# Performance work log

Measured on AMD Instinct MI355X. Metric: run time of the kernel, lower is better.

## Reference

```python
import jax, jax.numpy as jnp
import numpy as np


def _grid_sample_3d(vol, grid):
    """Trilinear 3D grid_sample, zero padding, align_corners=False (torch default).

    vol:  [B, C, D, H, W]
    grid: [B, P, 3] normalized coords in [-1, 1]; grid[...,0]->W axis,
          grid[...,1]->H axis, grid[...,2]->D axis (torch convention).
    returns [B, C, P]
    """
    B, C, D, H, W = vol.shape
    x = (grid[..., 0] + 1.0) * (W * 0.5) - 0.5
    y = (grid[..., 1] + 1.0) * (H * 0.5) - 0.5
    z = (grid[..., 2] + 1.0) * (D * 0.5) - 0.5
    x0, y0, z0 = jnp.floor(x), jnp.floor(y), jnp.floor(z)
    gather = jax.vmap(lambda v, zz, yy, xx: v[:, zz, yy, xx])  # per-batch gather -> [C, P]
    out = jnp.zeros((B, C, x.shape[1]), vol.dtype)
    for dz in (0.0, 1.0):
        for dy in (0.0, 1.0):
            for dx in (0.0, 1.0):
                xi, yi, zi = x0 + dx, y0 + dy, z0 + dz
                w = (1.0 - jnp.abs(x - xi)) * (1.0 - jnp.abs(y - yi)) * (1.0 - jnp.abs(z - zi))
                valid = (xi >= 0) & (xi < W) & (yi >= 0) & (yi < H) & (zi >= 0) & (zi < D)
                xc = jnp.clip(xi, 0, W - 1).astype(jnp.int32)
                yc = jnp.clip(yi, 0, H - 1).astype(jnp.int32)
                zc = jnp.clip(zi, 0, D - 1).astype(jnp.int32)
                vals = gather(vol, zc, yc, xc)  # [B, C, P]
                out = out + vals * jnp.where(valid, w, 0.0)[:, None, :]
    return out


def _offset_grid(xs, A, Wk):
    """xs: [N,3] sample points; A: [N,3,3]; Wk: [3,K] offset weights.
    Returns [N, K, 3] grid coords ordered (z_feat, y_feat, x_feat) as in the torch code."""
    off = jnp.einsum('nij,jk->nik', A, Wk)  # bmm with repeated weight -> [N,3,K]
    xf = xs[:, 2:3] + off[:, 0, :]
    yf = xs[:, 1:2] + off[:, 1, :]
    zf = xs[:, 0:1] + off[:, 2, :]
    return jnp.stack([zf, yf, xf], axis=-1)


def setup_inputs() -> dict:
    key = jax.random.key(0)
    k1, k2, k3, k4 = jax.random.split(key, 4)
    B, C, D, H, W = 2, 16, 96, 96, 96
    Feats, K = 512, 1024
    inp = jax.random.normal(k1, (B, C, D, H, W), jnp.float32)
    xyz_sample = jax.random.uniform(k2, (B, Feats, 3), jnp.float32, -1.0, 1.0)
    A = jax.random.normal(k3, (B * Feats, 3, 3), jnp.float32) * 0.1
    weight = jax.random.normal(k4, (6, K), jnp.float32) * 0.05  # xyz_off.weight
    return {"input": inp, "xyz_sample": xyz_sample, "A": A, "weight": weight}


def reference(input, xyz_sample, A, weight):
    B, Feats, _ = xyz_sample.shape
    C = input.shape[1]
    K = weight.shape[1]  # 1024
    xs = xyz_sample.reshape(B * Feats, 3)
    g1 = _offset_grid(xs, A, weight[:3]).reshape(B, Feats * K, 3)
    g2 = _offset_grid(xs, A, weight[3:]).reshape(B, Feats * K, 3)
    feats = _grid_sample_3d(input, g1) - _grid_sample_3d(input, g2)  # [B, C, Feats*K]
    return feats.reshape(B, C * Feats, K)
```

## Files before the change

### kernel.cpp

```cpp
#include <hip/hip_runtime.h>


#define NB 2
#define NC 16
#define NS 96
#define FEATS 512
#define NK 1024
#define KSPLIT 4
#define KSHIFT 2
#define KCHUNK (NK / KSPLIT)
#define DPASSES (KCHUNK / 128)

#define RVOX 8
#define VSTRIDE 48

#define TP 388

__device__ __forceinline__ unsigned int bfround(float f) {
  unsigned int u = __float_as_uint(f);
  return (u + 0x7fffu + ((u >> 16) & 1u)) >> 16;
}

__global__ __launch_bounds__(256) void transpose_bf16_kernel(
    const float* __restrict__ vol, unsigned short* __restrict__ volT) {
  int bid = blockIdx.x;
  int hq = bid % 24;
  int t = bid / 24;
  int d = t % NS;
  int b = t / NS;

  __shared__ float sm[NC * TP];
  int tid = threadIdx.x;

  const float4* v4 = (const float4*)vol;
#pragma unroll
  for (int j = 0; j < 6; j++) {
    int i = tid + 256 * j;
    int c = i / 96;
    int u = i - c * 96;
    size_t src = (size_t)((b * NC + c) * NS + d) * 2304 + hq * 96 + u;
    *(float4*)&sm[c * TP + u * 4] = v4[src];
  }
  __syncthreads();

  size_t dstb = ((size_t)(b * NS + d) * 9216 + (size_t)hq * 384) * NC;
#pragma unroll
  for (int j = 0; j < 3; j++) {
    int m = tid + 256 * j;
    int t16 = m >> 1;
    int ch = m & 1;
    unsigned int r[4];
#pragma unroll
    for (int q = 0; q < 4; q++) {
      float lo = sm[(ch * 8 + 2 * q) * TP + t16];
      float hi = sm[(ch * 8 + 2 * q + 1) * TP + t16];
      r[q] = bfround(lo) | (bfround(hi) << 16);
    }
    *(uint4*)(volT + dstb + (size_t)m * 8) = make_uint4(r[0], r[1], r[2], r[3]);
  }
}

#define BLO(v) __uint_as_float((v) << 16)
#define BHI(v) __uint_as_float((v) & 0xffff0000u)

__device__ __forceinline__ void tri_duo(
    const unsigned short* __restrict__ vg,
    size_t bbase,
    const unsigned char* __restrict__ sp,
    int ox0, int oy0, int oz0,
    float x, float y, float z, float sgn, float acc[8]) {
  float fx0 = floorf(x), fy0 = floorf(y), fz0 = floorf(z);
  int ix0 = (int)fx0, iy0 = (int)fy0, iz0 = (int)fz0;
  float tx = x - fx0, ty = y - fy0, tz = z - fz0;
  float wxa[2] = {1.0f - tx, tx};
  float wya[2] = {1.0f - ty, ty};
  float wza[2] = {1.0f - tz, tz};

  int lx0 = ix0 - ox0, ly0 = iy0 - oy0, lz0 = iz0 - oz0;
  bool fast = ((unsigned)lx0 < 7u) & ((unsigned)ly0 < 7u) & ((unsigned)lz0 < 7u);

  if (__builtin_expect(fast, 1)) {
#pragma unroll
    for (int dz = 0; dz < 2; dz++) {
      float wz = sgn * wza[dz];
#pragma unroll
      for (int dy = 0; dy < 2; dy++) {
        float wzy = wz * wya[dy];
        const unsigned char* rp =
            sp + (((lz0 + dz) * RVOX + (ly0 + dy)) * RVOX + lx0) * VSTRIDE;
#pragma unroll
        for (int dx = 0; dx < 2; dx++) {
          float w = wzy * wxa[dx];
          uint4 u = *(const uint4*)(rp + dx * VSTRIDE);
          acc[0] += w * BLO(u.x);
          acc[1] += w * BHI(u.x);
          acc[2] += w * BLO(u.y);
          acc[3] += w * BHI(u.y);
          acc[4] += w * BLO(u.z);
          acc[5] += w * BHI(u.z);
          acc[6] += w * BLO(u.w);
          acc[7] += w * BHI(u.w);
        }
      }
    }
  } else {
#pragma unroll
    for (int dz = 0; dz < 2; dz++) {
      int zc = iz0 + dz;
      if ((unsigned)zc >= (unsigned)NS) continue;
#pragma unroll
      for (int dy = 0; dy < 2; dy++) {
        int yc = iy0 + dy;
        if ((unsigned)yc >= (unsigned)NS) continue;
        size_t rowb = bbase + ((size_t)zc * NS + yc) * (NS * NC);
        float wzy = sgn * wza[dz] * wya[dy];
#pragma unroll
        for (int dx = 0; dx < 2; dx++) {
          int xc = ix0 + dx;
          if ((unsigned)xc >= (unsigned)NS) continue;
          float w = wzy * wxa[dx];
          uint4 u = *(const uint4*)(vg + rowb + (size_t)xc * NC);
          acc[0] += w * BLO(u.x);
          acc[1] += w * BHI(u.x);
          acc[2] += w * BLO(u.y);
          acc[3] += w * BHI(u.y);
          acc[4] += w * BLO(u.z);
          acc[5] += w * BHI(u.z);
          acc[6] += w * BLO(u.w);
          acc[7] += w * BHI(u.w);
        }
      }
    }
  }
}

__global__ __launch_bounds__(256) void sample_kernel_q(
    const unsigned short* __restrict__ volT,
    const float* __restrict__ xyz, const float* __restrict__ A,
    const float* __restrict__ weight, float* __restrict__ out) {
  __shared__ float wsm[6 * KCHUNK];
  __shared__ __align__(16) unsigned char stage[RVOX * RVOX * RVOX * VSTRIDE];

  int bid = blockIdx.x;
  int kseg = bid & (KSPLIT - 1);
  int n = bid >> KSHIFT;
  int b = n >> 9;
  int f = n & 511;
  int kbase = kseg * KCHUNK;

  for (int i = threadIdx.x; i < 6 * KCHUNK; i += 256)
    wsm[i] = weight[(i / KCHUNK) * NK + kbase + (i % KCHUNK)];

  const float* An = A + (size_t)n * 9;
  float a00 = An[0], a01 = An[1], a02 = An[2];
  float a10 = An[3], a11 = An[4], a12 = An[5];
  float a20 = An[6], a21 = An[7], a22 = An[8];
  const float* Xn = xyz + (size_t)n * 3;
  float bx = (Xn[0] + 1.0f) * 48.0f - 0.5f;
  float by = (Xn[1] + 1.0f) * 48.0f - 0.5f;
  float bz = (Xn[2] + 1.0f) * 48.0f - 0.5f;

  int ox0 = (int)floorf(bx) - 3;
  int oy0 = (int)floorf(by) - 3;
  int oz0 = (int)floorf(bz) - 3;

  size_t bbase = (size_t)b * (NS * NS * NS * NC);

  for (int v = threadIdx.x; v < RVOX * RVOX * RVOX; v += 256) {
    int dx = v & 7, dy = (v >> 3) & 7, dz = v >> 6;
    int xc = ox0 + dx, yc = oy0 + dy, zc = oz0 + dz;
    uint4 lo = make_uint4(0u, 0u, 0u, 0u);
    uint4 hi = make_uint4(0u, 0u, 0u, 0u);
    if (((unsigned)xc < (unsigned)NS) & ((unsigned)yc < (unsigned)NS) &
        ((unsigned)zc < (unsigned)NS)) {
      const uint4* g = (const uint4*)(volT + bbase +
                                      (((size_t)zc * NS + yc) * NS + xc) * NC);
      lo = g[0];
      hi = g[1];
    }
    unsigned char* p = stage + (size_t)v * VSTRIDE;
    *(uint4*)p = lo;
    *(uint4*)(p + 16) = hi;
  }
  __syncthreads();

  int duo = threadIdx.x & 1;
  int ksub = threadIdx.x >> 1;
  const unsigned short* vg = volT + duo * 8;
  const unsigned char* sp = stage + duo * 16;
  size_t obase = (size_t)b * (NC * FEATS * NK) +
                 (size_t)(duo * 8) * (FEATS * NK) + (size_t)f * NK + kbase;

  for (int pass = 0; pass < DPASSES; pass++) {
    int kl = pass * 128 + ksub;
    float w0 = wsm[kl];
    float w1 = wsm[KCHUNK + kl];
    float w2 = wsm[2 * KCHUNK + kl];
    float w3 = wsm[3 * KCHUNK + kl];
    float w4 = wsm[4 * KCHUNK + kl];
    float w5 = wsm[5 * KCHUNK + kl];

    float acc[8] = {0.0f, 0.0f, 0.0f, 0.0f, 0.0f, 0.0f, 0.0f, 0.0f};

    {
      float oz = a00 * w0 + a01 * w1 + a02 * w2;
      float oy = a10 * w0 + a11 * w1 + a12 * w2;
      float ox = a20 * w0 + a21 * w1 + a22 * w2;
      tri_duo(vg, bbase, sp, ox0, oy0, oz0, bx + ox * 48.0f, by + oy * 48.0f,
              bz + oz * 48.0f, 1.0f, acc);
    }
    {
      float oz = a00 * w3 + a01 * w4 + a02 * w5;
      float oy = a10 * w3 + a11 * w4 + a12 * w5;
      float ox = a20 * w3 + a21 * w4 + a22 * w5;
      tri_duo(vg, bbase, sp, ox0, oy0, oz0, bx + ox * 48.0f, by + oy * 48.0f,
              bz + oz * 48.0f, -1.0f, acc);
    }

    size_t o = obase + kl;
#pragma unroll
    for (int c = 0; c < 8; c++)
      out[o + (size_t)c * (FEATS * NK)] = acc[c];
  }
}

__global__ __launch_bounds__(256) void sample_kernel_fallback(
    const float* __restrict__ vol, const float* __restrict__ xyz,
    const float* __restrict__ A, const float* __restrict__ weight,
    float* __restrict__ out) {
  int n = blockIdx.x;
  int b = n >> 9;
  int f = n & 511;
  const float* An = A + (size_t)n * 9;
  float a00 = An[0], a01 = An[1], a02 = An[2];
  float a10 = An[3], a11 = An[4], a12 = An[5];
  float a20 = An[6], a21 = An[7], a22 = An[8];
  const float* Xn = xyz + (size_t)n * 3;
  float bx = (Xn[0] + 1.0f) * 48.0f - 0.5f;
  float by = (Xn[1] + 1.0f) * 48.0f - 0.5f;
  float bz = (Xn[2] + 1.0f) * 48.0f - 0.5f;
  size_t obase = (size_t)b * (NC * FEATS * NK) + (size_t)f * NK;

  for (int k = threadIdx.x; k < NK; k += 256) {
    float w0 = weight[k], w1 = weight[NK + k], w2 = weight[2 * NK + k];
    float w3 = weight[3 * NK + k], w4 = weight[4 * NK + k],
          w5 = weight[5 * NK + k];
    float acc[NC];
#pragma unroll
    for (int c = 0; c < NC; c++) acc[c] = 0.0f;
    for (int g = 0; g < 2; g++) {
      float u0 = g ? w3 : w0, u1 = g ? w4 : w1, u2 = g ? w5 : w2;
      float sgn = g ? -1.0f : 1.0f;
      float oz = a00 * u0 + a01 * u1 + a02 * u2;
      float oy = a10 * u0 + a11 * u1 + a12 * u2;
      float ox = a20 * u0 + a21 * u1 + a22 * u2;
      float x = bx + ox * 48.0f, y = by + oy * 48.0f, z = bz + oz * 48.0f;
      float fx0 = floorf(x), fy0 = floorf(y), fz0 = floorf(z);
      int ix0 = (int)fx0, iy0 = (int)fy0, iz0 = (int)fz0;
      float tx = x - fx0, ty = y - fy0, tz = z - fz0;
      float wxa[2] = {1.0f - tx, tx}, wya[2] = {1.0f - ty, ty},
            wza[2] = {1.0f - tz, tz};
      for (int dz = 0; dz < 2; dz++) {
        int zc = iz0 + dz;
        if ((unsigned)zc >= (unsigned)NS) continue;
        for (int dy = 0; dy < 2; dy++) {
          int yc = iy0 + dy;
          if ((unsigned)yc >= (unsigned)NS) continue;
          for (int dx = 0; dx < 2; dx++) {
            int xc = ix0 + dx;
            if ((unsigned)xc >= (unsigned)NS) continue;
            float w = sgn * wza[dz] * wya[dy] * wxa[dx];
            size_t base = (size_t)b * NC * NS * NS * NS +
                          (size_t)zc * NS * NS + (size_t)yc * NS + xc;
#pragma unroll
            for (int c = 0; c < NC; c++)
              acc[c] += w * vol[base + (size_t)c * (NS * NS * NS)];
          }
        }
      }
    }
#pragma unroll
    for (int c = 0; c < NC; c++)
      out[obase + (size_t)c * (FEATS * NK) + k] = acc[c];
  }
}

extern "C" void kernel_launch(void* const* d_in, const int* in_sizes, int n_in,
                              void* d_out, int out_size, void* d_ws,
                              size_t ws_size, hipStream_t stream) {
  const float* vol    = (const float*)d_in[0];
  const float* xyz    = (const float*)d_in[1];
  const float* A      = (const float*)d_in[2];
  const float* weight = (const float*)d_in[3];
  float* out = (float*)d_out;

  const size_t volT_bytes =
      (size_t)NB * NC * NS * NS * NS * sizeof(unsigned short);

  if (ws_size >= volT_bytes) {
    unsigned short* volT = (unsigned short*)d_ws;
    transpose_bf16_kernel<<<NB * NS * 24, 256, 0, stream>>>(vol, volT);
    sample_kernel_q<<<NB * FEATS * KSPLIT, 256, 0, stream>>>(volT, xyz, A,
                                                             weight, out);
  } else {
    sample_kernel_fallback<<<NB * FEATS, 256, 0, stream>>>(vol, xyz, A, weight,
                                                           out);
  }
}
```

Measured before the change: 223.9 us.

## Fuse volume transpose into sampler, staging bf16 neighborhood directly from fp32 input

Drops the separate full-volume transpose/bf16 conversion kernel. Each block now gathers its 8x8x8 voxel neighborhood straight from the channel-major fp32 volume, converts it to bf16 in shared memory, and falls back to fp32 global reads when a sample lands outside the stage. KSPLIT is halved to 2 so each block covers more K and amortizes staging, and the offset weights are loaded into registers instead of shared memory. The goal is to avoid the transpose's full-volume read and write; the cost is strided channel gathers (eight loads per voxel at stride NS^3) and fewer, longer blocks.

```diff
diff --git a/kernel.cpp b/kernel.cpp
--- a/kernel.cpp
+++ b/kernel.cpp
@@ -4,68 +4,26 @@
 #define NB 2
 #define NC 16
 #define NS 96
+#define NS3 (NS * NS * NS)
 #define FEATS 512
 #define NK 1024
-#define KSPLIT 4
-#define KSHIFT 2
+#define KSPLIT 2
 #define KCHUNK (NK / KSPLIT)
-#define DPASSES (KCHUNK / 128)
+#define PASSES 4
 
 #define RVOX 8
 #define VSTRIDE 48
-
-#define TP 388
 
 __device__ __forceinline__ unsigned int bfround(float f) {
   unsigned int u = __float_as_uint(f);
   return (u + 0x7fffu + ((u >> 16) & 1u)) >> 16;
 }
 
-__global__ __launch_bounds__(256) void transpose_bf16_kernel(
-    const float* __restrict__ vol, unsigned short* __restrict__ volT) {
-  int bid = blockIdx.x;
-  int hq = bid % 24;
-  int t = bid / 24;
-  int d = t % NS;
-  int b = t / NS;
-
-  __shared__ float sm[NC * TP];
-  int tid = threadIdx.x;
-
-  const float4* v4 = (const float4*)vol;
-#pragma unroll
-  for (int j = 0; j < 6; j++) {
-    int i = tid + 256 * j;
-    int c = i / 96;
-    int u = i - c * 96;
-    size_t src = (size_t)((b * NC + c) * NS + d) * 2304 + hq * 96 + u;
-    *(float4*)&sm[c * TP + u * 4] = v4[src];
-  }
-  __syncthreads();
-
-  size_t dstb = ((size_t)(b * NS + d) * 9216 + (size_t)hq * 384) * NC;
-#pragma unroll
-  for (int j = 0; j < 3; j++) {
-    int m = tid + 256 * j;
-    int t16 = m >> 1;
-    int ch = m & 1;
-    unsigned int r[4];
-#pragma unroll
-    for (int q = 0; q < 4; q++) {
-      float lo = sm[(ch * 8 + 2 * q) * TP + t16];
-      float hi = sm[(ch * 8 + 2 * q + 1) * TP + t16];
-      r[q] = bfround(lo) | (bfround(hi) << 16);
-    }
-    *(uint4*)(volT + dstb + (size_t)m * 8) = make_uint4(r[0], r[1], r[2], r[3]);
-  }
-}
-
 #define BLO(v) __uint_as_float((v) << 16)
 #define BHI(v) __uint_as_float((v) & 0xffff0000u)
 
 __device__ __forceinline__ void tri_duo(
-    const unsigned short* __restrict__ vg,
-    size_t bbase,
+    const float* __restrict__ vol, size_t cbase,
     const unsigned char* __restrict__ sp,
     int ox0, int oy0, int oz0,
     float x, float y, float z, float sgn, float acc[8]) {
@@ -112,93 +70,104 @@
       for (int dy = 0; dy < 2; dy++) {
         int yc = iy0 + dy;
         if ((unsigned)yc >= (unsigned)NS) continue;
-        size_t rowb = bbase + ((size_t)zc * NS + yc) * (NS * NC);
         float wzy = sgn * wza[dz] * wya[dy];
 #pragma unroll
         for (int dx = 0; dx < 2; dx++) {
           int xc = ix0 + dx;
           if ((unsigned)xc >= (unsigned)NS) continue;
           float w = wzy * wxa[dx];
-          uint4 u = *(const uint4*)(vg + rowb + (size_t)xc * NC);
-          acc[0] += w * BLO(u.x);
-          acc[1] += w * BHI(u.x);
-          acc[2] += w * BLO(u.y);
-          acc[3] += w * BHI(u.y);
-          acc[4] += w * BLO(u.z);
-          acc[5] += w * BHI(u.z);
-          acc[6] += w * BLO(u.w);
-          acc[7] += w * BHI(u.w);
+          const float* p = vol + cbase + (((size_t)zc * NS + yc) * NS + xc);
+#pragma unroll
+          for (int c = 0; c < 8; c++)
+            acc[c] += w * p[(size_t)c * NS3];
         }
       }
     }
   }
 }
 
-__global__ __launch_bounds__(256) void sample_kernel_q(
-    const unsigned short* __restrict__ volT,
-    const float* __restrict__ xyz, const float* __restrict__ A,
-    const float* __restrict__ weight, float* __restrict__ out) {
-  __shared__ float wsm[6 * KCHUNK];
+__global__ __launch_bounds__(256) void sample_fused(
+    const float* __restrict__ vol, const float* __restrict__ xyz,
+    const float* __restrict__ A, const float* __restrict__ weight,
+    float* __restrict__ out) {
   __shared__ __align__(16) unsigned char stage[RVOX * RVOX * RVOX * VSTRIDE];
 
   int bid = blockIdx.x;
   int kseg = bid & (KSPLIT - 1);
-  int n = bid >> KSHIFT;
+  int n = bid >> 1;
   int b = n >> 9;
   int f = n & 511;
   int kbase = kseg * KCHUNK;
-
-  for (int i = threadIdx.x; i < 6 * KCHUNK; i += 256)
-    wsm[i] = weight[(i / KCHUNK) * NK + kbase + (i % KCHUNK)];
+  int tid = threadIdx.x;
+
+  const float* Xn = xyz + (size_t)n * 3;
+  float bx = (Xn[0] + 1.0f) * 48.0f - 0.5f;
+  float by = (Xn[1] + 1.0f) * 48.0f - 0.5f;
+  float bz = (Xn[2] + 1.0f) * 48.0f - 0.5f;
+  int ox0 = (int)floorf(bx) - 3;
+  int oy0 = (int)floorf(by) - 3;
+  int oz0 = (int)floorf(bz) - 3;
+
+  int duo = tid & 1;
+  int ksub = tid >> 1;
+
+  float wreg[PASSES][6];
+#pragma unroll
+  for (int p = 0; p < PASSES; p++) {
+    int k = kbase + p * 128 + ksub;
+#pragma unroll
+    for (int q = 0; q < 6; q++) wreg[p][q] = weight[q * NK + k];
+  }
 
   const float* An = A + (size_t)n * 9;
   float a00 = An[0], a01 = An[1], a02 = An[2];
   float a10 = An[3], a11 = An[4], a12 = An[5];
   float a20 = An[6], a21 = An[7], a22 = An[8];
-  const float* Xn = xyz + (size_t)n * 3;
-  float bx = (Xn[0] + 1.0f) * 48.0f - 0.5f;
-  float by = (Xn[1] + 1.0f) * 48.0f - 0.5f;
-  float bz = (Xn[2] + 1.0f) * 48.0f - 0.5f;
-
-  int ox0 = (int)floorf(bx) - 3;
-  int oy0 = (int)floorf(by) - 3;
-  int oz0 = (int)floorf(bz) - 3;
-
-  size_t bbase = (size_t)b * (NS * NS * NS * NC);
-
-  for (int v = threadIdx.x; v < RVOX * RVOX * RVOX; v += 256) {
-    int dx = v & 7, dy = (v >> 3) & 7, dz = v >> 6;
-    int xc = ox0 + dx, yc = oy0 + dy, zc = oz0 + dz;
-    uint4 lo = make_uint4(0u, 0u, 0u, 0u);
-    uint4 hi = make_uint4(0u, 0u, 0u, 0u);
+
+  size_t vb = (size_t)b * NC * NS3;
+#pragma unroll
+  for (int j = 0; j < 4; j++) {
+    int w = tid + 256 * j;
+    int half = w & 1;
+    int v = w >> 1;
+    int xg = v & 7, yg = (v >> 3) & 7, zg = v >> 6;
+    int xc = ox0 + xg, yc = oy0 + yg, zc = oz0 + zg;
+    uint4 r = make_uint4(0u, 0u, 0u, 0u);
     if (((unsigned)xc < (unsigned)NS) & ((unsigned)yc < (unsigned)NS) &
         ((unsigned)zc < (unsigned)NS)) {
-      const uint4* g = (const uint4*)(volT + bbase +
-                                      (((size_t)zc * NS + yc) * NS + xc) * NC);
-      lo = g[0];
-      hi = g[1];
-    }
-    unsigned char* p = stage + (size_t)v * VSTRIDE;
-    *(uint4*)p = lo;
-    *(uint4*)(p + 16) = hi;
+      const float* p = vol + vb + (size_t)(half * 8) * NS3 +
+                       (((size_t)zc * NS + yc) * NS + xc);
+      float f0 = p[0];
+      float f1 = p[NS3];
+      float f2 = p[2 * NS3];
+      float f3 = p[3 * NS3];
+      float f4 = p[4 * NS3];
+      float f5 = p[5 * NS3];
+      float f6 = p[6 * NS3];
+      float f7 = p[7 * NS3];
+      r.x = bfround(f0) | (bfround(f1) << 16);
+      r.y = bfround(f2) | (bfround(f3) << 16);
+      r.z = bfround(f4) | (bfround(f5) << 16);
+      r.w = bfround(f6) | (bfround(f7) << 16);
+    }
+    *(uint4*)(stage + (size_t)v * VSTRIDE + half * 16) = r;
   }
   __syncthreads();
 
-  int duo = threadIdx.x & 1;
-  int ksub = threadIdx.x >> 1;
-  const unsigned short* vg = volT + duo * 8;
   const unsigned char* sp = stage + duo * 16;
+  size_t cbase = ((size_t)b * NC + duo * 8) * NS3;
   size_t obase = (size_t)b * (NC * FEATS * NK) +
                  (size_t)(duo * 8) * (FEATS * NK) + (size_t)f * NK + kbase;
 
-  for (int pass = 0; pass < DPASSES; pass++) {
+#pragma unroll
+  for (int pass = 0; pass < PASSES; pass++) {
     int kl = pass * 128 + ksub;
-    float w0 = wsm[kl];
-    float w1 = wsm[KCHUNK + kl];
-    float w2 = wsm[2 * KCHUNK + kl];
-    float w3 = wsm[3 * KCHUNK + kl];
-    float w4 = wsm[4 * KCHUNK + kl];
-    float w5 = wsm[5 * KCHUNK + kl];
+    float w0 = wreg[pass][0];
+    float w1 = wreg[pass][1];
+    float w2 = wreg[pass][2];
+    float w3 = wreg[pass][3];
+    float w4 = wreg[pass][4];
+    float w5 = wreg[pass][5];
 
     float acc[8] = {0.0f, 0.0f, 0.0f, 0.0f, 0.0f, 0.0f, 0.0f, 0.0f};
 
@@ -206,14 +175,14 @@
       float oz = a00 * w0 + a01 * w1 + a02 * w2;
       float oy = a10 * w0 + a11 * w1 + a12 * w2;
       float ox = a20 * w0 + a21 * w1 + a22 * w2;
-      tri_duo(vg, bbase, sp, ox0, oy0, oz0, bx + ox * 48.0f, by + oy * 48.0f,
+      tri_duo(vol, cbase, sp, ox0, oy0, oz0, bx + ox * 48.0f, by + oy * 48.0f,
               bz + oz * 48.0f, 1.0f, acc);
     }
     {
       float oz = a00 * w3 + a01 * w4 + a02 * w5;
       float oy = a10 * w3 + a11 * w4 + a12 * w5;
       float ox = a20 * w3 + a21 * w4 + a22 * w5;
-      tri_duo(vg, bbase, sp, ox0, oy0, oz0, bx + ox * 48.0f, by + oy * 48.0f,
+      tri_duo(vol, cbase, sp, ox0, oy0, oz0, bx + ox * 48.0f, by + oy * 48.0f,
               bz + oz * 48.0f, -1.0f, acc);
     }
 
@@ -221,67 +190,6 @@
 #pragma unroll
     for (int c = 0; c < 8; c++)
       out[o + (size_t)c * (FEATS * NK)] = acc[c];
-  }
-}
-
-__global__ __launch_bounds__(256) void sample_kernel_fallback(
-    const float* __restrict__ vol, const float* __restrict__ xyz,
-    const float* __restrict__ A, const float* __restrict__ weight,
-    float* __restrict__ out) {
-  int n = blockIdx.x;
-  int b = n >> 9;
-  int f = n & 511;
-  const float* An = A + (size_t)n * 9;
-  float a00 = An[0], a01 = An[1], a02 = An[2];
-  float a10 = An[3], a11 = An[4], a12 = An[5];
-  float a20 = An[6], a21 = An[7], a22 = An[8];
-  const float* Xn = xyz + (size_t)n * 3;
-  float bx = (Xn[0] + 1.0f) * 48.0f - 0.5f;
-  float by = (Xn[1] + 1.0f) * 48.0f - 0.5f;
-  float bz = (Xn[2] + 1.0f) * 48.0f - 0.5f;
-  size_t obase = (size_t)b * (NC * FEATS * NK) + (size_t)f * NK;
-
-  for (int k = threadIdx.x; k < NK; k += 256) {
-    float w0 = weight[k], w1 = weight[NK + k], w2 = weight[2 * NK + k];
-    float w3 = weight[3 * NK + k], w4 = weight[4 * NK + k],
-          w5 = weight[5 * NK + k];
-    float acc[NC];
-#pragma unroll
-    for (int c = 0; c < NC; c++) acc[c] = 0.0f;
-    for (int g = 0; g < 2; g++) {
-      float u0 = g ? w3 : w0, u1 = g ? w4 : w1, u2 = g ? w5 : w2;
-      float sgn = g ? -1.0f : 1.0f;
-      float oz = a00 * u0 + a01 * u1 + a02 * u2;
-      float oy = a10 * u0 + a11 * u1 + a12 * u2;
-      float ox = a20 * u0 + a21 * u1 + a22 * u2;
-      float x = bx + ox * 48.0f, y = by + oy * 48.0f, z = bz + oz * 48.0f;
-      float fx0 = floorf(x), fy0 = floorf(y), fz0 = floorf(z);
-      int ix0 = (int)fx0, iy0 = (int)fy0, iz0 = (int)fz0;
-      float tx = x - fx0, ty = y - fy0, tz = z - fz0;
-      float wxa[2] = {1.0f - tx, tx}, wya[2] = {1.0f - ty, ty},
-            wza[2] = {1.0f - tz, tz};
-      for (int dz = 0; dz < 2; dz++) {
-        int zc = iz0 + dz;
-        if ((unsigned)zc >= (unsigned)NS) continue;
-        for (int dy = 0; dy < 2; dy++) {
-          int yc = iy0 + dy;
-          if ((unsigned)yc >= (unsigned)NS) continue;
-          for (int dx = 0; dx < 2; dx++) {
-            int xc = ix0 + dx;
-            if ((unsigned)xc >= (unsigned)NS) continue;
-            float w = sgn * wza[dz] * wya[dy] * wxa[dx];
-            size_t base = (size_t)b * NC * NS * NS * NS +
-                          (size_t)zc * NS * NS + (size_t)yc * NS + xc;
-#pragma unroll
-            for (int c = 0; c < NC; c++)
-              acc[c] += w * vol[base + (size_t)c * (NS * NS * NS)];
-          }
-        }
-      }
-    }
-#pragma unroll
-    for (int c = 0; c < NC; c++)
-      out[obase + (size_t)c * (FEATS * NK) + k] = acc[c];
   }
 }
 
@@ -294,16 +202,6 @@
   const float* weight = (const float*)d_in[3];
   float* out = (float*)d_out;
 
-  const size_t volT_bytes =
-      (size_t)NB * NC * NS * NS * NS * sizeof(unsigned short);
-
-  if (ws_size >= volT_bytes) {
-    unsigned short* volT = (unsigned short*)d_ws;
-    transpose_bf16_kernel<<<NB * NS * 24, 256, 0, stream>>>(vol, volT);
-    sample_kernel_q<<<NB * FEATS * KSPLIT, 256, 0, stream>>>(volT, xyz, A,
-                                                             weight, out);
-  } else {
-    sample_kernel_fallback<<<NB * FEATS, 256, 0, stream>>>(vol, xyz, A, weight,
-                                                           out);
-  }
-}
+  sample_fused<<<NB * FEATS * KSPLIT, 256, 0, stream>>>(vol, xyz, A, weight,
+                                                        out);
+}
```

Result: faster. 200.0 us (-10.7%).
